# Kernel optimization log

Measured on AMD Instinct MI355X. Metric: run time of the kernel, lower is better.

Reference implementation:

```python
import jax, jax.numpy as jnp
import numpy as np


def setup_inputs() -> dict:
    key = jax.random.key(0)
    k0, k1, k2, k3 = jax.random.split(key, 4)
    B, H, W, C, h = 2, 64, 64, 256, 8
    N = H * W
    # per-pixel, per-head (dy, dx) match offsets; a few pixels of displacement
    max_offset = jax.random.normal(k0, (B, N, h, 2), dtype=jnp.float32) * 4.0
    q = jax.random.normal(k1, (B, N, C), dtype=jnp.float32)
    k = jax.random.normal(k2, (B, N, C), dtype=jnp.float32)
    v = jax.random.normal(k3, (B, N, C), dtype=jnp.float32)
    return {"max_offset": max_offset, "q": q, "k": k, "v": v,
            "H": H, "W": W, "r_h": 3, "r_w": 3}


def reference(max_offset, q, k, v, H, W, r_h, r_w):
    """MatchAttention fused forward (l1_norm, scale=1.0).

    Each query pixel (y,x), head g attends to a (2*r_h+1)x(2*r_w+1) window
    centered at (y,x) + round(max_offset[...,g]), clamped to the image.
    Similarity is the negative L1 distance between q and gathered k.
    Returns (output [B,N,C], attn_out [B,N,h,K]).
    """
    B, N, C = q.shape
    h = max_offset.shape[2]
    Ch = C // h
    scale = 1.0
    attn_type = "l1_norm"  # fixed; 'l2_norm' would use squared distance

    # window deltas, K = (2*r_h+1)*(2*r_w+1)
    dy = jnp.arange(-r_h, r_h + 1)
    dx = jnp.arange(-r_w, r_w + 1)
    gy, gx = jnp.meshgrid(dy, dx, indexing="ij")
    ddy, ddx = gy.reshape(-1), gx.reshape(-1)  # [K]

    ys = (jnp.arange(N) // W)[None, :, None]  # [1,N,1]
    xs = (jnp.arange(N) % W)[None, :, None]

    off = jnp.round(max_offset).astype(jnp.int32)  # [B,N,h,2] (dy,dx)
    cy = ys + off[..., 0]                          # [B,N,h] window center
    cx = xs + off[..., 1]
    py = jnp.clip(cy[..., None] + ddy, 0, H - 1)   # [B,N,h,K]
    px = jnp.clip(cx[..., None] + ddx, 0, W - 1)
    idx = py * W + px                              # flat pixel index, [B,N,h,K]

    # split heads and move head axis forward: [B,h,N,Ch]
    qh = q.reshape(B, N, h, Ch).transpose(0, 2, 1, 3)
    kh = k.reshape(B, N, h, Ch).transpose(0, 2, 1, 3)
    vh = v.reshape(B, N, h, Ch).transpose(0, 2, 1, 3)
    idx_t = idx.transpose(0, 2, 1, 3)              # [B,h,N,K]

    # gather windows: [B,h,N,K,Ch]
    gather = jax.vmap(jax.vmap(lambda tbl, i: tbl[i]))
    kg = gather(kh, idx_t)
    vg = gather(vh, idx_t)

    # negative L1 distance similarity, softmax over window
    sim = -scale * jnp.abs(qh[:, :, :, None, :] - kg).sum(-1)  # [B,h,N,K]
    attn = jax.nn.softmax(sim, axis=-1)

    out = jnp.einsum("bhnk,bhnkc->bhnc", attn, vg)
    output = out.transpose(0, 2, 1, 3).reshape(B, N, C)
    attn_out = attn.transpose(0, 2, 1, 3)          # [B,N,h,K]
    return output, attn_out
```

## Files before the change

### kernel.cpp

```cpp
#include <hip/hip_runtime.h>
#include <math.h>

constexpr int B = 2, H = 64, W = 64, C = 256, NH = 8, CH = 32;
constexpr int R = 3, KW = 7, KK = 49, N = H * W;
constexpr int ECH = 4;
constexpr int PIX_PER_BLK = 32;

__global__ void match_attn_kernel(
    const float* __restrict__ moff, const float* __restrict__ qp,
    const float* __restrict__ kp, const float* __restrict__ vp,
    float* __restrict__ outp, float* __restrict__ attnp) {
  const int t = threadIdx.x;
  const int e8 = t & 7;
  const int p = t >> 3;

  const int xcd = blockIdx.x & 7;
  const int rest = blockIdx.x >> 3;
  const int bg = xcd * 2 + (rest >> 7);
  const int slot = rest & 127;
  const int y = slot >> 1;
  const int x = (slot & 1) * PIX_PER_BLK + p;
  const int g = bg & 7;
  const int b = bg >> 3;
  const int n = y * W + x;

  const float2 off = *(const float2*)(moff + ((size_t)(b * N + n) * NH + g) * 2);
  const int cy = y + (int)rintf(off.x);
  const int cx = x + (int)rintf(off.y);

  const int chn = g * CH + e8 * ECH;
  const float4 q0 = *(const float4*)(qp + (size_t)(b * N + n) * C + chn);

  const float* kb = kp + (size_t)b * N * C + chn;
  const float* vb = vp + (size_t)b * N * C + chn;
  float* attn_px = attnp + ((size_t)(b * N + n) * NH + g) * KK;

  float4 acc = {0.f, 0.f, 0.f, 0.f};
  float denom = 0.f;

  for (int iy = 0; iy < KW; ++iy) {
    int py = cy + iy - R;
    py = min(max(py, 0), H - 1);
    const float* krow = kb + (size_t)(py * W) * C;
    const float* vrow = vb + (size_t)(py * W) * C;
#pragma unroll
    for (int ix = 0; ix < KW; ++ix) {
      int px = cx + ix - R;
      px = min(max(px, 0), W - 1);
      const float4 k0 = *(const float4*)(krow + (size_t)px * C);
      const float4 v0 = *(const float4*)(vrow + (size_t)px * C);
      float s = fabsf(q0.x - k0.x) + fabsf(q0.y - k0.y) +
                fabsf(q0.z - k0.z) + fabsf(q0.w - k0.w);
      s += __shfl_xor(s, 1);
      s += __shfl_xor(s, 2);
      s += __shfl_xor(s, 4);
      const float e = __expf(-s);
      denom += e;
      if (ix == e8) attn_px[iy * KW + ix] = e;
      acc.x += e * v0.x; acc.y += e * v0.y;
      acc.z += e * v0.z; acc.w += e * v0.w;
    }
  }
  const float inv = 1.0f / denom;

  float4 o;
  o.x = acc.x * inv; o.y = acc.y * inv; o.z = acc.z * inv; o.w = acc.w * inv;
  *(float4*)(outp + (size_t)(b * N + n) * C + chn) = o;

  if (e8 < KW) {
    for (int iy = 0; iy < KW; ++iy) {
      const int kk = iy * KW + e8;
      attn_px[kk] = attn_px[kk] * inv;
    }
  }
}

extern "C" void kernel_launch(void* const* d_in, const int* in_sizes, int n_in,
                              void* d_out, int out_size, void* d_ws, size_t ws_size,
                              hipStream_t stream) {
  const float* moff = (const float*)d_in[0];
  const float* q    = (const float*)d_in[1];
  const float* k    = (const float*)d_in[2];
  const float* v    = (const float*)d_in[3];
  float* out  = (float*)d_out;
  float* attn = out + (size_t)B * N * C;

  const int grid = B * NH * N / PIX_PER_BLK;
  match_attn_kernel<<<grid, 256, 0, stream>>>(moff, q, k, v, out, attn);
}
```

Measured before the change: 134.4 us.

## Split attention into score pass, shared-memory softmax, and weighted V pass

```diff
diff --git a/kernel.cpp b/kernel.cpp
--- a/kernel.cpp
+++ b/kernel.cpp
@@ -4,12 +4,15 @@
 constexpr int B = 2, H = 64, W = 64, C = 256, NH = 8, CH = 32;
 constexpr int R = 3, KW = 7, KK = 49, N = H * W;
 constexpr int ECH = 4;
-constexpr int PIX_PER_BLK = 32;
+constexpr int PIX = 32;
 
-__global__ void match_attn_kernel(
+__global__ void __launch_bounds__(256) match_attn_kernel(
     const float* __restrict__ moff, const float* __restrict__ qp,
     const float* __restrict__ kp, const float* __restrict__ vp,
     float* __restrict__ outp, float* __restrict__ attnp) {
+  __shared__ __align__(16) float part4[PIX][KK][4];
+  __shared__ __align__(16) float wbuf[PIX][52];
+
   const int t = threadIdx.x;
   const int e8 = t & 7;
   const int p = t >> 3;
@@ -19,7 +22,7 @@
   const int bg = xcd * 2 + (rest >> 7);
   const int slot = rest & 127;
   const int y = slot >> 1;
-  const int x = (slot & 1) * PIX_PER_BLK + p;
+  const int x = (slot & 1) * PIX + p;
   const int g = bg & 7;
   const int b = bg >> 3;
   const int n = y * W + x;
@@ -30,49 +33,67 @@
 
   const int chn = g * CH + e8 * ECH;
   const float4 q0 = *(const float4*)(qp + (size_t)(b * N + n) * C + chn);
-
   const float* kb = kp + (size_t)b * N * C + chn;
   const float* vb = vp + (size_t)b * N * C + chn;
+
+  for (int iy = 0; iy < KW; ++iy) {
+    const int py = min(max(cy + iy - R, 0), H - 1);
+    const float* krow = kb + (size_t)(py * W) * C;
+#pragma unroll
+    for (int ix = 0; ix < KW; ++ix) {
+      const int px = min(max(cx + ix - R, 0), W - 1);
+      const float4 k0 = *(const float4*)(krow + (size_t)px * C);
+      float s = fabsf(q0.x - k0.x) + fabsf(q0.y - k0.y) +
+                fabsf(q0.z - k0.z) + fabsf(q0.w - k0.w);
+      s += __shfl_xor(s, 1);
+      if ((e8 & 1) == 0) part4[p][iy * KW + ix][e8 >> 1] = s;
+    }
+  }
+  __syncthreads();
+
+  float ev[7];
+  float d = 0.f;
+#pragma unroll
+  for (int j = 0; j < 7; ++j) {
+    const int kk = e8 + 8 * j;
+    if (kk < KK) {
+      const float4 pa = *(const float4*)&part4[p][kk][0];
+      const float e = __expf(-(pa.x + pa.y + pa.z + pa.w));
+      ev[j] = e;
+      d += e;
+    }
+  }
+  d += __shfl_xor(d, 1);
+  d += __shfl_xor(d, 2);
+  d += __shfl_xor(d, 4);
+  const float inv = 1.0f / d;
+
   float* attn_px = attnp + ((size_t)(b * N + n) * NH + g) * KK;
+#pragma unroll
+  for (int j = 0; j < 7; ++j) {
+    const int kk = e8 + 8 * j;
+    if (kk < KK) {
+      const float w = ev[j] * inv;
+      wbuf[p][kk] = w;
+      attn_px[kk] = w;
+    }
+  }
+  __syncthreads();
 
   float4 acc = {0.f, 0.f, 0.f, 0.f};
-  float denom = 0.f;
-
   for (int iy = 0; iy < KW; ++iy) {
-    int py = cy + iy - R;
-    py = min(max(py, 0), H - 1);
-    const float* krow = kb + (size_t)(py * W) * C;
+    const int py = min(max(cy + iy - R, 0), H - 1);
     const float* vrow = vb + (size_t)(py * W) * C;
 #pragma unroll
     for (int ix = 0; ix < KW; ++ix) {
-      int px = cx + ix - R;
-      px = min(max(px, 0), W - 1);
-      const float4 k0 = *(const float4*)(krow + (size_t)px * C);
+      const int px = min(max(cx + ix - R, 0), W - 1);
       const float4 v0 = *(const float4*)(vrow + (size_t)px * C);
-      float s = fabsf(q0.x - k0.x) + fabsf(q0.y - k0.y) +
-                fabsf(q0.z - k0.z) + fabsf(q0.w - k0.w);
-      s += __shfl_xor(s, 1);
-      s += __shfl_xor(s, 2);
-      s += __shfl_xor(s, 4);
-      const float e = __expf(-s);
-      denom += e;
-      if (ix == e8) attn_px[iy * KW + ix] = e;
-      acc.x += e * v0.x; acc.y += e * v0.y;
-      acc.z += e * v0.z; acc.w += e * v0.w;
+      const float w = wbuf[p][iy * KW + ix];
+      acc.x += w * v0.x; acc.y += w * v0.y;
+      acc.z += w * v0.z; acc.w += w * v0.w;
     }
   }
-  const float inv = 1.0f / denom;
-
-  float4 o;
-  o.x = acc.x * inv; o.y = acc.y * inv; o.z = acc.z * inv; o.w = acc.w * inv;
-  *(float4*)(outp + (size_t)(b * N + n) * C + chn) = o;
-
-  if (e8 < KW) {
-    for (int iy = 0; iy < KW; ++iy) {
-      const int kk = iy * KW + e8;
-      attn_px[kk] = attn_px[kk] * inv;
-    }
-  }
+  *(float4*)(outp + (size_t)(b * N + n) * C + chn) = acc;
 }
 
 extern "C" void kernel_launch(void* const* d_in, const int* in_sizes, int n_in,
@@ -85,6 +106,6 @@
   float* out  = (float*)d_out;
   float* attn = out + (size_t)B * N * C;
 
-  const int grid = B * NH * N / PIX_PER_BLK;
+  const int grid = B * NH * N / PIX;
   match_attn_kernel<<<grid, 256, 0, stream>>>(moff, q, k, v, out, attn);
 }
```

After: 123.8 us. 1.09x faster.
